# Optimization experiments

Hardware: AMD Instinct MI355X
Metric: run time of the kernel (lower is better)

Reference implementation:

```python
import jax, jax.numpy as jnp
import numpy as np

DIM = 5120
NUM_HEADS = 40
HEAD_DIM = DIM // NUM_HEADS
EPS = 1e-6


def rms_norm(x, g):
    # RMSNorm over last dim in fp32 for stability
    xf = x.astype(jnp.float32)
    inv = jax.lax.rsqrt(jnp.mean(xf * xf, axis=-1, keepdims=True) + EPS)
    return (xf * inv).astype(x.dtype) * g


def setup_inputs() -> dict:
    key = jax.random.key(0)
    ks = jax.random.split(key, 12)
    B, S, L = 1, 4096, 512
    inp = {
        "hidden_cond": jax.random.normal(ks[0], (B, S, DIM), jnp.float32),
        "hidden_uncond": jax.random.normal(ks[1], (B, S, DIM), jnp.float32),
        "context_cond": jax.random.normal(ks[2], (B, L, DIM), jnp.float32),
        "context_uncond": jax.random.normal(ks[3], (B, L, DIM), jnp.float32),
        # parameters (torch nn.Linear: y = x @ W.T + b)
        "Wq": jax.random.normal(ks[4], (DIM, DIM), jnp.float32) * (DIM ** -0.5),
        "bq": jnp.zeros((DIM,), jnp.float32),
        "Wkv": jax.random.normal(ks[5], (2 * DIM, DIM), jnp.float32) * (DIM ** -0.5),
        "bkv": jnp.zeros((2 * DIM,), jnp.float32),
        "gq": jnp.ones((DIM,), jnp.float32),
        "gk": jnp.ones((DIM,), jnp.float32),
        "Wo": jax.random.normal(ks[6], (DIM, DIM), jnp.float32) * (DIM ** -0.5),
        "bo": jnp.zeros((DIM,), jnp.float32),
    }
    return inp


def reference(hidden_cond, hidden_uncond, context_cond, context_uncond,
              Wq, bq, Wkv, bkv, gq, gk, Wo, bo):
    H, Dh = NUM_HEADS, HEAD_DIM
    scale = Dh ** -0.5

    hidden = jnp.concatenate([hidden_cond, hidden_uncond], axis=0)   # [2B, S, D]
    context = jnp.concatenate([context_cond, context_uncond], axis=0)  # [2B, L, D]
    CB, S, D = hidden.shape
    L = context.shape[1]

    q = hidden @ Wq.T + bq                    # [2B, S, D]
    q = rms_norm(q, gq)
    q = q.reshape(CB, S, H, Dh).transpose(0, 2, 1, 3)  # [2B, H, S, Dh]

    kv = context @ Wkv.T + bkv                # [2B, L, 2D]
    kv = kv.reshape(CB, L, 2, H, Dh).transpose(2, 0, 3, 1, 4)  # [2,2B,H,L,Dh]
    k, v = kv[0], kv[1]

    k_flat = k.transpose(0, 2, 1, 3).reshape(CB, L, D)
    k_flat = rms_norm(k_flat, gk)
    k = k_flat.reshape(CB, L, H, Dh).transpose(0, 2, 1, 3)  # [2B, H, L, Dh]

    attn = jnp.einsum('bhsd,bhld->bhsl', q, k) * scale
    attn = jax.nn.softmax(attn.astype(jnp.float32), axis=-1).astype(q.dtype)
    out = jnp.einsum('bhsl,bhld->bhsd', attn, v)            # [2B, H, S, Dh]
    out = out.transpose(0, 2, 1, 3).reshape(CB, S, D)
    out = out @ Wo.T + bo

    out_cond, out_uncond = jnp.split(out, 2, axis=0)
    return (out_cond, out_uncond)
```

## Files before the change

kernel.cpp:

```cpp
#include <hip/hip_runtime.h>
#include <hip/hip_bf16.h>
#include <cstdint>
#include <cstddef>

#define DIM 5120
#define NH 40
#define HD 128
#define S_LEN 4096
#define L_LEN 512
#define CBATCH 2
#define MQ (CBATCH*S_LEN)
#define ML (CBATCH*L_LEN)

typedef unsigned short ushort_t;
typedef __bf16 bf16x8 __attribute__((ext_vector_type(8)));
typedef float f32x4 __attribute__((ext_vector_type(4)));
typedef float f32x16 __attribute__((ext_vector_type(16)));

__device__ __forceinline__ ushort_t f2bf(float f) {
  union { float f; unsigned u; } c; c.f = f;
  unsigned r = c.u + 0x7fffu + ((c.u >> 16) & 1u);
  return (ushort_t)(r >> 16);
}

__device__ __forceinline__ void load_lds16(const void* g, void* l) {
  __builtin_amdgcn_global_load_lds(
      (const __attribute__((address_space(1))) void*)g,
      (__attribute__((address_space(3))) void*)l, 16, 0, 0);
}

__global__ __launch_bounds__(256) void cvt_f32_bf16(const float* __restrict__ in,
                                                    ushort_t* __restrict__ out, int n4) {
  int i = blockIdx.x * 256 + threadIdx.x;
  if (i >= n4) return;
  float4 v = *(const float4*)(in + 4ull * (size_t)i);
  ushort4 o;
  o.x = f2bf(v.x); o.y = f2bf(v.y); o.z = f2bf(v.z); o.w = f2bf(v.w);
  *(ushort4*)(out + 4ull * (size_t)i) = o;
}

template <int OUT_F32>
__device__ __forceinline__ void gemm_core(const ushort_t* __restrict__ Ab,
                                          const ushort_t* __restrict__ Bb,
                                          const float* __restrict__ bias,
                                          void* __restrict__ Cout,
                                          int N, size_t m0, size_t n0,
                                          char* ldsc) {
  const int tid = threadIdx.x;
  const int lane = tid & 63, w = tid >> 6;
  const int g = lane >> 4, c = lane & 15;
  const int wm = w >> 2, wn = w & 3;
  constexpr int K = DIM;
  constexpr int NT = K >> 6;

  const int srow = tid >> 2;
  const int sgq  = (tid & 3) ^ (((tid >> 5) & 1) << 1);
  const size_t rb0 = (size_t)srow * K + (size_t)sgq * 8;
  const size_t rb1 = rb0 + (size_t)128 * K;
  const int d0 = tid * 16;

  int offA[8], offB[4];
#pragma unroll
  for (int m = 0; m < 8; ++m) {
    int row = wm * 128 + m * 16 + c;
    offA[m] = row * 64 + ((g * 16) ^ ((row & 8) << 2));
  }
#pragma unroll
  for (int n = 0; n < 4; ++n) {
    int row = wn * 64 + n * 16 + c;
    offB[n] = row * 64 + ((g * 16) ^ ((row & 8) << 2));
  }

  auto STAGE = [&](int tIdx, int j, int dOff) {
    const size_t kof = (size_t)tIdx * 64 + (size_t)((j >> 1) << 5);
    const ushort_t* gsrc = ((j & 1) ? Ab : Bb) + kof;
    char* db = ldsc + dOff;
    load_lds16(gsrc + rb0, db + d0);
    load_lds16(gsrc + rb1, db + 8192 + d0);
  };
  auto nx = [](int x) { return (x + 16384 == 147456) ? 0 : x + 16384; };

  f32x4 acc[8][4] = {};

#pragma unroll
  for (int h = 0; h < 8; ++h) STAGE(h >> 2, h & 3, h * 16384);
  asm volatile("s_waitcnt vmcnt(8)" ::: "memory");
  __builtin_amdgcn_s_barrier();

  int rd = 0;
  int sOff = 131072;
  for (int t = 0; t < NT; ++t) {
    const int r0 = rd, r1 = nx(r0), r2 = nx(r1), r3 = nx(r2);
    bf16x8 a[4], a2[4], b[4];
#pragma unroll
    for (int m = 0; m < 4; ++m) a[m] = *(const bf16x8*)(ldsc + r1 + offA[m]);
#pragma unroll
    for (int n = 0; n < 4; ++n) b[n] = *(const bf16x8*)(ldsc + r0 + offB[n]);
    if (t < NT - 2) { STAGE(t + 2, 0, sOff); sOff = nx(sOff); }
    __builtin_amdgcn_s_barrier();
    asm volatile("s_waitcnt lgkmcnt(0)" ::: "memory");
    __builtin_amdgcn_sched_barrier(0);
    __builtin_amdgcn_s_setprio(1);
#pragma unroll
    for (int m = 0; m < 4; ++m)
#pragma unroll
      for (int n = 0; n < 4; ++n)
        acc[m][n] = __builtin_amdgcn_mfma_f32_16x16x32_bf16(a[m], b[n], acc[m][n], 0, 0, 0);
    __builtin_amdgcn_s_setprio(0);
    __builtin_amdgcn_s_barrier();
#pragma unroll
    for (int m = 0; m < 4; ++m) a2[m] = *(const bf16x8*)(ldsc + r1 + offA[4 + m]);
    if (t < NT - 2) { STAGE(t + 2, 1, sOff); sOff = nx(sOff); }
    __builtin_amdgcn_s_barrier();
    asm volatile("s_waitcnt lgkmcnt(0)" ::: "memory");
    __builtin_amdgcn_sched_barrier(0);
    __builtin_amdgcn_s_setprio(1);
#pragma unroll
    for (int m = 0; m < 4; ++m)
#pragma unroll
      for (int n = 0; n < 4; ++n)
        acc[4 + m][n] = __builtin_amdgcn_mfma_f32_16x16x32_bf16(a2[m], b[n], acc[4 + m][n], 0, 0, 0);
    __builtin_amdgcn_s_setprio(0);
    __builtin_amdgcn_s_barrier();
#pragma unroll
    for (int m = 0; m < 4; ++m) a[m] = *(const bf16x8*)(ldsc + r3 + offA[m]);
#pragma unroll
    for (int n = 0; n < 4; ++n) b[n] = *(const bf16x8*)(ldsc + r2 + offB[n]);
    if (t < NT - 2) { STAGE(t + 2, 2, sOff); sOff = nx(sOff); }
    __builtin_amdgcn_s_barrier();
    asm volatile("s_waitcnt lgkmcnt(0)" ::: "memory");
    __builtin_amdgcn_sched_barrier(0);
    __builtin_amdgcn_s_setprio(1);
#pragma unroll
    for (int m = 0; m < 4; ++m)
#pragma unroll
      for (int n = 0; n < 4; ++n)
        acc[m][n] = __builtin_amdgcn_mfma_f32_16x16x32_bf16(a[m], b[n], acc[m][n], 0, 0, 0);
    __builtin_amdgcn_s_setprio(0);
    __builtin_amdgcn_s_barrier();
#pragma unroll
    for (int m = 0; m < 4; ++m) a2[m] = *(const bf16x8*)(ldsc + r3 + offA[4 + m]);
    if (t < NT - 2) { STAGE(t + 2, 3, sOff); sOff = nx(sOff); }
    __builtin_amdgcn_s_barrier();
    asm volatile("s_waitcnt lgkmcnt(0)" ::: "memory");
    __builtin_amdgcn_sched_barrier(0);
    __builtin_amdgcn_s_setprio(1);
#pragma unroll
    for (int m = 0; m < 4; ++m)
#pragma unroll
      for (int n = 0; n < 4; ++n)
        acc[4 + m][n] = __builtin_amdgcn_mfma_f32_16x16x32_bf16(a2[m], b[n], acc[4 + m][n], 0, 0, 0);
    __builtin_amdgcn_s_setprio(0);
    if (t < NT - 2)       asm volatile("s_waitcnt vmcnt(6)" ::: "memory");
    else if (t == NT - 2) asm volatile("s_waitcnt vmcnt(0)" ::: "memory");
    __builtin_amdgcn_s_barrier();
    rd = nx(r3);
  }

#pragma unroll
  for (int m = 0; m < 8; ++m) {
#pragma unroll
    for (int n = 0; n < 4; ++n) {
      size_t gm = m0 + wm * 128 + m * 16 + g * 4;
      size_t gn = n0 + wn * 64 + n * 16 + c;
      float bn = bias[gn];
#pragma unroll
      for (int r = 0; r < 4; ++r) {
        float v = acc[m][n][r] + bn;
        if (OUT_F32) ((float*)Cout)[(gm + r) * (size_t)N + gn] = v;
        else         ((ushort_t*)Cout)[(gm + r) * (size_t)N + gn] = f2bf(v);
      }
    }
  }
}

__global__ __launch_bounds__(512, 2) void gemm_fused_qkv(
    const ushort_t* __restrict__ hbf, const ushort_t* __restrict__ wq,
    const ushort_t* __restrict__ cbf, const ushort_t* __restrict__ wkv,
    const float* __restrict__ bq, const float* __restrict__ bkv,
    ushort_t* __restrict__ qb, ushort_t* __restrict__ kvb) {
  __shared__ ushort_t lds[73728];
  char* ldsc = (char*)lds;
  const int nwg = 800;
  int bid = blockIdx.x;
  bid = (bid & 7) * (nwg >> 3) + (bid >> 3);
  if (bid < 640) {
    const int tm = bid / 20, tn = bid % 20;
    const size_t m0 = (size_t)tm * 256, n0 = (size_t)tn * 256;
    gemm_core<0>(hbf + m0 * DIM, wq + n0 * DIM, bq, qb, DIM, m0, n0, ldsc);
  } else {
    const int e = bid - 640;
    const int tm = e / 40, tn = e % 40;
    const size_t m0 = (size_t)tm * 256, n0 = (size_t)tn * 256;
    gemm_core<0>(cbf + m0 * DIM, wkv + n0 * DIM, bkv, kvb, 2 * DIM, m0, n0, ldsc);
  }
}

__global__ __launch_bounds__(512, 2) void gemm_out(
    const ushort_t* __restrict__ A, const ushort_t* __restrict__ W,
    const float* __restrict__ bias, float* __restrict__ C) {
  __shared__ ushort_t lds[73728];
  char* ldsc = (char*)lds;
  const int nwg = 640;
  int bid = blockIdx.x;
  bid = (bid & 7) * (nwg >> 3) + (bid >> 3);
  const int tm = bid / 20, tn = bid % 20;
  const size_t m0 = (size_t)tm * 256, n0 = (size_t)tn * 256;
  gemm_core<1>(A + m0 * DIM, W + n0 * DIM, bias, C, DIM, m0, n0, ldsc);
}

__global__ __launch_bounds__(256) void rmsnorm_rows(ushort_t* __restrict__ x,
                                                    const float* __restrict__ gw,
                                                    int ncols, int stride, float oscale) {
  const int row = blockIdx.x;
  ushort_t* p = x + (size_t)row * stride;
  const int tid = threadIdx.x;
  const int nch = ncols >> 3;
  float ss = 0.f;
  for (int ci = tid; ci < nch; ci += 256) {
    bf16x8 v = *(const bf16x8*)(p + ci * 8);
#pragma unroll
    for (int j = 0; j < 8; ++j) { float f = (float)v[j]; ss += f * f; }
  }
#pragma unroll
  for (int off = 1; off < 64; off <<= 1) ss += __shfl_xor(ss, off);
  __shared__ float sred[4];
  if ((tid & 63) == 0) sred[tid >> 6] = ss;
  __syncthreads();
  float tot = sred[0] + sred[1] + sred[2] + sred[3];
  float inv = rsqrtf(tot / (float)ncols + 1e-6f) * oscale;
  for (int ci = tid; ci < nch; ci += 256) {
    bf16x8 v = *(const bf16x8*)(p + ci * 8);
    bf16x8 ov;
#pragma unroll
    for (int j = 0; j < 8; ++j) {
      float f = (float)v[j];
      ushort_t ob = f2bf(f * inv * gw[ci * 8 + j]);
      ov[j] = *(__bf16*)&ob;
    }
    *(bf16x8*)(p + ci * 8) = ov;
  }
}

__global__ __launch_bounds__(256) void transpose_v(const ushort_t* __restrict__ kv,
                                                   ushort_t* __restrict__ vt) {
  const int bh = blockIdx.y, b = bh / NH, h = bh % NH;
  const int l0 = blockIdx.x * 32;
  const ushort_t* src = kv + (size_t)b * L_LEN * (2 * DIM) + DIM + (size_t)h * HD;
  ushort_t* dst = vt + (size_t)bh * HD * L_LEN;
  __shared__ ushort_t tile[32][HD + 16];
  const int tid = threadIdx.x;
#pragma unroll
  for (int i = 0; i < 2; ++i) {
    int gid = i * 256 + tid;
    int r = gid >> 4, ce = (gid & 15) << 3;
    *(bf16x8*)(&tile[r][ce]) = *(const bf16x8*)(src + (size_t)(l0 + r) * (2 * DIM) + ce);
  }
  __syncthreads();
#pragma unroll
  for (int i = 0; i < 2; ++i) {
    int gid = i * 256 + tid;
    int d = gid >> 2, le = (gid & 3) << 3;
    bf16x8 v;
#pragma unroll
    for (int j = 0; j < 8; ++j) v[j] = *(__bf16*)&tile[le + j][d];
    *(bf16x8*)(dst + (size_t)d * L_LEN + l0 + le) = v;
  }
}

__global__ __launch_bounds__(256) void attn_fwd(const ushort_t* __restrict__ q,
                                                const ushort_t* __restrict__ kv,
                                                const ushort_t* __restrict__ vt,
                                                ushort_t* __restrict__ out) {
  const int bh = blockIdx.y, b = bh / NH, h = bh % NH;
  const int tid = threadIdx.x, w = tid >> 6, lane = tid & 63;
  const int lq = lane & 31, hi = lane >> 5;
  const int qr0 = blockIdx.x * 128 + w * 32;

  __shared__ ushort_t sK[2][4096];
  __shared__ ushort_t sV[2][4096];

  const int skl = tid >> 3, skc = tid & 7;
  const ushort_t* kgsrc = kv + ((size_t)b * L_LEN + skl) * (2 * DIM)
                             + (size_t)h * HD + skc * 16;
  ushort_t* kd0 = &sK[0][(skc * 2) * 256 + skl * 8];
  ushort_t* kd1 = &sK[0][(skc * 2 + 1) * 256 + skl * 8];
  const int svd = tid >> 1, svh = tid & 1;
  const ushort_t* vgsrc = vt + (size_t)bh * HD * L_LEN + (size_t)svd * L_LEN + svh * 16;
  ushort_t* vd0 = &sV[0][(svh * 2) * 1024 + svd * 8];
  ushort_t* vd1 = &sV[0][(svh * 2 + 1) * 1024 + svd * 8];

  const ushort_t* qrow = q + ((size_t)b * S_LEN + qr0 + lq) * DIM + (size_t)h * HD + hi * 8;
  bf16x8 qf[8];
#pragma unroll
  for (int ks = 0; ks < 8; ++ks) qf[ks] = *(const bf16x8*)(qrow + ks * 16);

  f32x16 o[4];
#pragma unroll
  for (int ch = 0; ch < 4; ++ch) o[ch] = 0.f;
  float m = -1e30f, lsum = 0.f;

  {
    uint4 ka = *(const uint4*)kgsrc;
    uint4 kb = *(const uint4*)(kgsrc + 8);
    uint4 va = *(const uint4*)vgsrc;
    uint4 vb = *(const uint4*)(vgsrc + 8);
    *(uint4*)kd0 = ka; *(uint4*)kd1 = kb;
    *(uint4*)vd0 = va; *(uint4*)vd1 = vb;
  }
  __syncthreads();

  const int NT = L_LEN / 32;
  int buf = 0;
  for (int t = 0; t < NT; ++t) {
    uint4 ka, kb, va, vb;
    if (t + 1 < NT) {
      const ushort_t* kg = kgsrc + (size_t)(t + 1) * 32 * (2 * DIM);
      const ushort_t* vg = vgsrc + (t + 1) * 32;
      ka = *(const uint4*)kg; kb = *(const uint4*)(kg + 8);
      va = *(const uint4*)vg; vb = *(const uint4*)(vg + 8);
    }

    const ushort_t* kbuf = sK[buf];
    const ushort_t* vbuf = sV[buf];

    f32x16 sv = 0.f;
#pragma unroll
    for (int ks = 0; ks < 8; ++ks) {
      bf16x8 kf = *(const bf16x8*)(kbuf + (ks * 2 + hi) * 256 + lq * 8);
      sv = __builtin_amdgcn_mfma_f32_32x32x16_bf16(kf, qf[ks], sv, 0, 0, 0);
    }
    float pm = fmaxf(fmaxf(fmaxf(sv[0], sv[1]), fmaxf(sv[2], sv[3])),
                     fmaxf(fmaxf(sv[4], sv[5]), fmaxf(sv[6], sv[7])));
    pm = fmaxf(pm, fmaxf(fmaxf(fmaxf(sv[8], sv[9]), fmaxf(sv[10], sv[11])),
                         fmaxf(fmaxf(sv[12], sv[13]), fmaxf(sv[14], sv[15]))));
    pm = fmaxf(pm, __shfl_xor(pm, 32));
    if (__ballot(pm > m + 8.0f)) {
      float mn = fmaxf(m, pm);
      float al = __builtin_amdgcn_exp2f(m - mn);
      lsum *= al;
      m = mn;
#pragma unroll
      for (int r = 0; r < 16; ++r) {
        float ar = __shfl(al, (r & 3) + 8 * (r >> 2) + 4 * hi);
        o[0][r] *= ar; o[1][r] *= ar; o[2][r] *= ar; o[3][r] *= ar;
      }
    }
    float p[16]; float ls = 0.f;
#pragma unroll
    for (int r = 0; r < 16; ++r) { p[r] = __builtin_amdgcn_exp2f(sv[r] - m); ls += p[r]; }
    ls += __shfl_xor(ls, 32);
    lsum += ls;
    bf16x8 pa[2];
#pragma unroll
    for (int ks = 0; ks < 2; ++ks) {
      unsigned w0 = (unsigned)f2bf(p[8 * ks + 0]) | ((unsigned)f2bf(p[8 * ks + 1]) << 16);
      unsigned w1 = (unsigned)f2bf(p[8 * ks + 2]) | ((unsigned)f2bf(p[8 * ks + 3]) << 16);
      unsigned w2 = (unsigned)f2bf(p[8 * ks + 4]) | ((unsigned)f2bf(p[8 * ks + 5]) << 16);
      unsigned w3 = (unsigned)f2bf(p[8 * ks + 6]) | ((unsigned)f2bf(p[8 * ks + 7]) << 16);
      unsigned e0 = __shfl_xor((int)w0, 32), e1 = __shfl_xor((int)w1, 32);
      unsigned e2 = __shfl_xor((int)w2, 32), e3 = __shfl_xor((int)w3, 32);
      unsigned d0 = hi ? e2 : w0, d1 = hi ? e3 : w1;
      unsigned d2 = hi ? w2 : e0, d3 = hi ? w3 : e1;
      unsigned tmp[4] = {d0, d1, d2, d3};
      pa[ks] = *(const bf16x8*)tmp;
    }
#pragma unroll
    for (int ch = 0; ch < 4; ++ch) {
#pragma unroll
      for (int ks = 0; ks < 2; ++ks) {
        bf16x8 vf = *(const bf16x8*)(vbuf + (ks * 2 + hi) * 1024 + (ch * 32 + lq) * 8);
        o[ch] = __builtin_amdgcn_mfma_f32_32x32x16_bf16(pa[ks], vf, o[ch], 0, 0, 0);
      }
    }

    if (t + 1 < NT) {
      const int nb = buf ^ 1;
      *(uint4*)(kd0 + nb * 4096) = ka; *(uint4*)(kd1 + nb * 4096) = kb;
      *(uint4*)(vd0 + nb * 4096) = va; *(uint4*)(vd1 + nb * 4096) = vb;
    }
    __syncthreads();
    buf ^= 1;
  }

  float inv[16];
#pragma unroll
  for (int r = 0; r < 16; ++r) {
    float lr = __shfl(lsum, (r & 3) + 8 * (r >> 2) + 4 * hi);
    inv[r] = 1.0f / lr;
  }
  ushort_t* ob = out + ((size_t)b * S_LEN + qr0) * DIM + (size_t)h * HD;
#pragma unroll
  for (int ch = 0; ch < 4; ++ch)
#pragma unroll
    for (int r = 0; r < 16; ++r) {
      int row = (r & 3) + 8 * (r >> 2) + 4 * hi;
      ob[(size_t)row * DIM + ch * 32 + lq] = f2bf(o[ch][r] * inv[r]);
    }
}

extern "C" void kernel_launch(void* const* d_in, const int* in_sizes, int n_in,
                              void* d_out, int out_size, void* d_ws, size_t ws_size,
                              hipStream_t stream) {
  (void)in_sizes; (void)n_in; (void)out_size; (void)ws_size;
  const float* hidden_c = (const float*)d_in[0];
  const float* hidden_u = (const float*)d_in[1];
  const float* ctx_c    = (const float*)d_in[2];
  const float* ctx_u    = (const float*)d_in[3];
  const float* Wq  = (const float*)d_in[4];
  const float* bq  = (const float*)d_in[5];
  const float* Wkv = (const float*)d_in[6];
  const float* bkv = (const float*)d_in[7];
  const float* gq  = (const float*)d_in[8];
  const float* gk  = (const float*)d_in[9];
  const float* Wo  = (const float*)d_in[10];
  const float* bo  = (const float*)d_in[11];

  char* ws = (char*)d_ws;
  size_t off = 0;
  auto alloc = [&](size_t bytes) {
    char* p = ws + off; off += (bytes + 255) & ~(size_t)255; return p;
  };
  ushort_t* hbf  = (ushort_t*)alloc((size_t)MQ * DIM * 2);
  ushort_t* cbf  = (ushort_t*)alloc((size_t)ML * DIM * 2);
  ushort_t* wqb  = (ushort_t*)alloc((size_t)DIM * DIM * 2);
  ushort_t* wkvb = (ushort_t*)alloc((size_t)2 * DIM * DIM * 2);
  ushort_t* kvb  = (ushort_t*)alloc((size_t)ML * 2 * DIM * 2);
  ushort_t* vtb  = (ushort_t*)alloc((size_t)CBATCH * NH * HD * L_LEN * 2);
  ushort_t* qb   = (ushort_t*)d_out;

  auto cvt = [&](const float* in, ushort_t* o, size_t n) {
    int n4 = (int)(n >> 2);
    cvt_f32_bf16<<<dim3((n4 + 255) / 256), dim3(256), 0, stream>>>(in, o, n4);
  };
  cvt(hidden_c, hbf, (size_t)S_LEN * DIM);
  cvt(hidden_u, hbf + (size_t)S_LEN * DIM, (size_t)S_LEN * DIM);
  cvt(ctx_c, cbf, (size_t)L_LEN * DIM);
  cvt(ctx_u, cbf + (size_t)L_LEN * DIM, (size_t)L_LEN * DIM);
  cvt(Wq, wqb, (size_t)DIM * DIM);
  cvt(Wkv, wkvb, (size_t)2 * DIM * DIM);

  gemm_fused_qkv<<<dim3(800), dim3(512), 0, stream>>>(
      hbf, wqb, cbf, wkvb, bq, bkv, qb, kvb);
  cvt(Wo, wqb, (size_t)DIM * DIM);

  const float qscale = 0.08838834764831845f * 1.4426950408889634f;
  rmsnorm_rows<<<dim3(MQ), dim3(256), 0, stream>>>(qb, gq, DIM, DIM, qscale);
  rmsnorm_rows<<<dim3(ML), dim3(256), 0, stream>>>(kvb, gk, DIM, 2 * DIM, 1.0f);
  transpose_v<<<dim3(L_LEN / 32, CBATCH * NH), dim3(256), 0, stream>>>(kvb, vtb);

  attn_fwd<<<dim3(S_LEN / 128, CBATCH * NH), dim3(256), 0, stream>>>(qb, kvb, vtb, hbf);

  gemm_out<<<dim3(640), dim3(512), 0, stream>>>(hbf, wqb, bo, (float*)d_out);
}
```

Measured before the change: 1.371 ms.

## Fuse RMSNorm scaling into attention loads and remap GEMM tile order

The RMSNorm kernels now only compute per-row inverse RMS factors into small buffers, and the gain and inverse scaling is applied inside the attention kernel when Q fragments and K tiles are loaded. This removes a full read-modify-write pass over the Q and K activations. In exchange it adds per-element normalisation arithmetic and extra small loads in the attention loop. Separately, the GEMM block-to-tile mapping is changed to walk M-major (tm = bid & 31), which alters L2 reuse of weight tiles.

After: 1.546 ms. 12.8% more time.

```diff
diff --git a/kernel.cpp b/kernel.cpp
--- a/kernel.cpp
+++ b/kernel.cpp
@@ -17,6 +17,9 @@
 typedef float f32x4 __attribute__((ext_vector_type(4)));
 typedef float f32x16 __attribute__((ext_vector_type(16)));
 
+__device__ __forceinline__ float bf2f(ushort_t u) {
+  union { unsigned u; float f; } c; c.u = ((unsigned)u) << 16; return c.f;
+}
 __device__ __forceinline__ ushort_t f2bf(float f) {
   union { float f; unsigned u; } c; c.f = f;
   unsigned r = c.u + 0x7fffu + ((c.u >> 16) & 1u);
@@ -27,6 +30,14 @@
   __builtin_amdgcn_global_load_lds(
       (const __attribute__((address_space(1))) void*)g,
       (__attribute__((address_space(3))) void*)l, 16, 0, 0);
+}
+
+__device__ __forceinline__ uint4 norm8(uint4 v, float s, const float* g) {
+  union { uint4 u; ushort_t h[8]; } in, out;
+  in.u = v;
+#pragma unroll
+  for (int e = 0; e < 8; ++e) out.h[e] = f2bf(bf2f(in.h[e]) * s * g[e]);
+  return out.u;
 }
 
 __global__ __launch_bounds__(256) void cvt_f32_bf16(const float* __restrict__ in,
@@ -181,16 +192,15 @@
     ushort_t* __restrict__ qb, ushort_t* __restrict__ kvb) {
   __shared__ ushort_t lds[73728];
   char* ldsc = (char*)lds;
-  const int nwg = 800;
   int bid = blockIdx.x;
-  bid = (bid & 7) * (nwg >> 3) + (bid >> 3);
+  bid = (bid & 7) * 100 + (bid >> 3);
   if (bid < 640) {
-    const int tm = bid / 20, tn = bid % 20;
+    const int tm = bid & 31, tn = bid >> 5;
     const size_t m0 = (size_t)tm * 256, n0 = (size_t)tn * 256;
     gemm_core<0>(hbf + m0 * DIM, wq + n0 * DIM, bq, qb, DIM, m0, n0, ldsc);
   } else {
     const int e = bid - 640;
-    const int tm = e / 40, tn = e % 40;
+    const int tm = e & 3, tn = e >> 2;
     const size_t m0 = (size_t)tm * 256, n0 = (size_t)tn * 256;
     gemm_core<0>(cbf + m0 * DIM, wkv + n0 * DIM, bkv, kvb, 2 * DIM, m0, n0, ldsc);
   }
@@ -201,19 +211,18 @@
     const float* __restrict__ bias, float* __restrict__ C) {
   __shared__ ushort_t lds[73728];
   char* ldsc = (char*)lds;
-  const int nwg = 640;
   int bid = blockIdx.x;
-  bid = (bid & 7) * (nwg >> 3) + (bid >> 3);
-  const int tm = bid / 20, tn = bid % 20;
+  bid = (bid & 7) * 80 + (bid >> 3);
+  const int tm = bid & 31, tn = bid >> 5;
   const size_t m0 = (size_t)tm * 256, n0 = (size_t)tn * 256;
   gemm_core<1>(A + m0 * DIM, W + n0 * DIM, bias, C, DIM, m0, n0, ldsc);
 }
 
-__global__ __launch_bounds__(256) void rmsnorm_rows(ushort_t* __restrict__ x,
-                                                    const float* __restrict__ gw,
-                                                    int ncols, int stride, float oscale) {
+__global__ __launch_bounds__(256) void rowinv(const ushort_t* __restrict__ x,
+                                              float* __restrict__ out,
+                                              int ncols, int stride, float oscale) {
   const int row = blockIdx.x;
-  ushort_t* p = x + (size_t)row * stride;
+  const ushort_t* p = x + (size_t)row * stride;
   const int tid = threadIdx.x;
   const int nch = ncols >> 3;
   float ss = 0.f;
@@ -227,18 +236,9 @@
   __shared__ float sred[4];
   if ((tid & 63) == 0) sred[tid >> 6] = ss;
   __syncthreads();
-  float tot = sred[0] + sred[1] + sred[2] + sred[3];
-  float inv = rsqrtf(tot / (float)ncols + 1e-6f) * oscale;
-  for (int ci = tid; ci < nch; ci += 256) {
-    bf16x8 v = *(const bf16x8*)(p + ci * 8);
-    bf16x8 ov;
-#pragma unroll
-    for (int j = 0; j < 8; ++j) {
-      float f = (float)v[j];
-      ushort_t ob = f2bf(f * inv * gw[ci * 8 + j]);
-      ov[j] = *(__bf16*)&ob;
-    }
-    *(bf16x8*)(p + ci * 8) = ov;
+  if (tid == 0) {
+    float tot = sred[0] + sred[1] + sred[2] + sred[3];
+    out[row] = rsqrtf(tot / (float)ncols + 1e-6f) * oscale;
   }
 }
 
@@ -271,6 +271,10 @@
 __global__ __launch_bounds__(256) void attn_fwd(const ushort_t* __restrict__ q,
                                                 const ushort_t* __restrict__ kv,
                                                 const ushort_t* __restrict__ vt,
+                                                const float* __restrict__ invq,
+                                                const float* __restrict__ invk,
+                                                const float* __restrict__ gq,
+                                                const float* __restrict__ gk,
                                                 ushort_t* __restrict__ out) {
   const int bh = blockIdx.y, b = bh / NH, h = bh % NH;
   const int tid = threadIdx.x, w = tid >> 6, lane = tid & 63;
@@ -290,10 +294,28 @@
   ushort_t* vd0 = &sV[0][(svh * 2) * 1024 + svd * 8];
   ushort_t* vd1 = &sV[0][(svh * 2 + 1) * 1024 + svd * 8];
 
+  float gkv[16];
+  {
+    const float* gp = gk + h * HD + skc * 16;
+#pragma unroll
+    for (int e = 0; e < 16; ++e) gkv[e] = gp[e];
+  }
+
   const ushort_t* qrow = q + ((size_t)b * S_LEN + qr0 + lq) * DIM + (size_t)h * HD + hi * 8;
+  const float iq = invq[(size_t)b * S_LEN + qr0 + lq];
   bf16x8 qf[8];
 #pragma unroll
-  for (int ks = 0; ks < 8; ++ks) qf[ks] = *(const bf16x8*)(qrow + ks * 16);
+  for (int ks = 0; ks < 8; ++ks) {
+    bf16x8 r = *(const bf16x8*)(qrow + ks * 16);
+    const float* gp = gq + h * HD + ks * 16 + hi * 8;
+    bf16x8 nq;
+#pragma unroll
+    for (int e = 0; e < 8; ++e) {
+      ushort_t ob_ = f2bf((float)r[e] * iq * gp[e]);
+      nq[e] = *(__bf16*)&ob_;
+    }
+    qf[ks] = nq;
+  }
 
   f32x16 o[4];
 #pragma unroll
@@ -301,8 +323,9 @@
   float m = -1e30f, lsum = 0.f;
 
   {
-    uint4 ka = *(const uint4*)kgsrc;
-    uint4 kb = *(const uint4*)(kgsrc + 8);
+    float ik = invk[(size_t)b * L_LEN + skl];
+    uint4 ka = norm8(*(const uint4*)kgsrc, ik, gkv);
+    uint4 kb = norm8(*(const uint4*)(kgsrc + 8), ik, gkv + 8);
     uint4 va = *(const uint4*)vgsrc;
     uint4 vb = *(const uint4*)(vgsrc + 8);
     *(uint4*)kd0 = ka; *(uint4*)kd1 = kb;
@@ -314,11 +337,13 @@
   int buf = 0;
   for (int t = 0; t < NT; ++t) {
     uint4 ka, kb, va, vb;
+    float ik = 0.f;
     if (t + 1 < NT) {
       const ushort_t* kg = kgsrc + (size_t)(t + 1) * 32 * (2 * DIM);
       const ushort_t* vg = vgsrc + (t + 1) * 32;
       ka = *(const uint4*)kg; kb = *(const uint4*)(kg + 8);
       va = *(const uint4*)vg; vb = *(const uint4*)(vg + 8);
+      ik = invk[(size_t)b * L_LEN + (t + 1) * 32 + skl];
     }
 
     const ushort_t* kbuf = sK[buf];
@@ -376,6 +401,8 @@
 
     if (t + 1 < NT) {
       const int nb = buf ^ 1;
+      ka = norm8(ka, ik, gkv);
+      kb = norm8(kb, ik, gkv + 8);
       *(uint4*)(kd0 + nb * 4096) = ka; *(uint4*)(kd1 + nb * 4096) = kb;
       *(uint4*)(vd0 + nb * 4096) = va; *(uint4*)(vd1 + nb * 4096) = vb;
     }
@@ -427,6 +454,8 @@
   ushort_t* wkvb = (ushort_t*)alloc((size_t)2 * DIM * DIM * 2);
   ushort_t* kvb  = (ushort_t*)alloc((size_t)ML * 2 * DIM * 2);
   ushort_t* vtb  = (ushort_t*)alloc((size_t)CBATCH * NH * HD * L_LEN * 2);
+  float*    invq = (float*)alloc((size_t)MQ * 4);
+  float*    invk = (float*)alloc((size_t)ML * 4);
   ushort_t* qb   = (ushort_t*)d_out;
 
   auto cvt = [&](const float* in, ushort_t* o, size_t n) {
@@ -445,11 +474,12 @@
   cvt(Wo, wqb, (size_t)DIM * DIM);
 
   const float qscale = 0.08838834764831845f * 1.4426950408889634f;
-  rmsnorm_rows<<<dim3(MQ), dim3(256), 0, stream>>>(qb, gq, DIM, DIM, qscale);
-  rmsnorm_rows<<<dim3(ML), dim3(256), 0, stream>>>(kvb, gk, DIM, 2 * DIM, 1.0f);
+  rowinv<<<dim3(MQ), dim3(256), 0, stream>>>(qb, invq, DIM, DIM, qscale);
+  rowinv<<<dim3(ML), dim3(256), 0, stream>>>(kvb, invk, DIM, 2 * DIM, 1.0f);
   transpose_v<<<dim3(L_LEN / 32, CBATCH * NH), dim3(256), 0, stream>>>(kvb, vtb);
 
-  attn_fwd<<<dim3(S_LEN / 128, CBATCH * NH), dim3(256), 0, stream>>>(qb, kvb, vtb, hbf);
+  attn_fwd<<<dim3(S_LEN / 128, CBATCH * NH), dim3(256), 0, stream>>>(
+      qb, kvb, vtb, invq, invk, gq, gk, hbf);
 
   gemm_out<<<dim3(640), dim3(512), 0, stream>>>(hbf, wqb, bo, (float*)d_out);
 }
```
